# Kernel tuning notes

Hardware: AMD Instinct MI355X
Metric: run time of the kernel (lower is better)

The kernel has to match this reference:

```python
import jax, jax.numpy as jnp
import numpy as np

W_DIST = 1.0
W_ANGLE = 1.0
EPS = 1e-12


def setup_inputs() -> dict:
    key = jax.random.key(0)
    k1, k2, k3 = jax.random.split(key, 3)
    B, C = 384, 512
    return {
        "feat_s": jax.random.normal(k1, (B, C), dtype=jnp.float32),
        "feat_t": jax.random.normal(k2, (B, C), dtype=jnp.float32),
        "labels": jax.random.randint(k3, (B,), 0, C, dtype=jnp.int64),
    }


def _pdist(feat):
    # Euclidean pairwise distances with zeroed diagonal (matches RKD.pdist).
    sq = jnp.sum(feat * feat, axis=1)                      # [B]
    prod = feat @ feat.T                                   # [B,B]
    d = jnp.clip(sq[None, :] + sq[:, None] - 2.0 * prod, EPS, None)
    d = jnp.sqrt(d)
    B = feat.shape[0]
    return d * (1.0 - jnp.eye(B, dtype=feat.dtype))


def _norm_pdist(feat):
    d = _pdist(feat)
    pos = d > 0
    mean_pos = jnp.sum(jnp.where(pos, d, 0.0)) / jnp.maximum(jnp.sum(pos), 1)
    return d / mean_pos


def _smooth_l1(x, y):
    a = jnp.abs(x - y)
    return jnp.mean(jnp.where(a < 1.0, 0.5 * a * a, a - 0.5))


def _angle_gram(feat):
    # vd[i, j] = feat[j] - feat[i], normalized along feature dim (F.normalize eps=1e-12)
    vd = feat[None, :, :] - feat[:, None, :]               # [B,B,C]
    nrm = jnp.sqrt(jnp.sum(vd * vd, axis=2, keepdims=True))
    vd = vd / jnp.maximum(nrm, EPS)
    return jnp.einsum('bic,bjc->bij', vd, vd)              # [B,B,B]


def _rkd(feat_s, feat_t):
    dist_loss = _smooth_l1(_norm_pdist(feat_s), _norm_pdist(feat_t))
    angle_loss = _smooth_l1(_angle_gram(feat_s), _angle_gram(feat_t))
    return W_DIST * dist_loss + W_ANGLE * angle_loss


def reference(feat_s, feat_t, labels):
    # hard CE loss (mean reduction)
    logp = jax.nn.log_softmax(feat_s, axis=-1)
    hard_loss = -jnp.mean(logp[jnp.arange(feat_s.shape[0]), labels])
    # soft RKD loss; teacher detached as in the torch code
    soft_loss = _rkd(feat_s, jax.lax.stop_gradient(feat_t))
    return hard_loss + soft_loss
```

## Files before the change

### kernel.cpp

```cpp
#include <hip/hip_runtime.h>
#include <hip/hip_bf16.h>
#include <math.h>

#define B 384
#define C 512
#define NPAIR (B * B)
#define NOFF  (B * (B - 1))

#define T16  24
#define UP16 300
#define T64  6
#define UP64 21
#define NBG  32
#define NANG (UP64 * NBG)

#define HARD_OFF 0
#define DSUM_OFF 384
#define ANG_OFF  984
#define DIST_OFF 1656
#define SQS_OFF  1680
#define SQT_OFF  2064
#define PS_OFF   2448
#define PT_OFF   (PS_OFF + NPAIR)

typedef __attribute__((ext_vector_type(8))) short short8;
typedef __attribute__((ext_vector_type(4))) float floatx4;

__device__ __forceinline__ float blk_sum(float v, float* s4, int t) {
#pragma unroll
  for (int off = 32; off > 0; off >>= 1) v += __shfl_down(v, off, 64);
  if ((t & 63) == 0) s4[t >> 6] = v;
  __syncthreads();
  float r = s4[0] + s4[1] + s4[2] + s4[3];
  __syncthreads();
  return r;
}

__device__ __forceinline__ short bfc(float x) {
  __hip_bfloat16 h = __float2bfloat16(x);
  return __builtin_bit_cast(short, h);
}

__global__ __launch_bounds__(256, 4) void k_pre(const float* __restrict__ fs,
                                                const float* __restrict__ ft,
                                                const int* __restrict__ lab,
                                                float* __restrict__ ws) {
  int t = threadIdx.x;
  if (blockIdx.x < 96) {
    int wv = t >> 6, lane = t & 63;
    int r = blockIdx.x * 4 + wv;
    const float* xs = fs + r * C;
    const float* xt = ft + r * C;
    float4 a0 = *(const float4*)&xs[lane * 8];
    float4 a1 = *(const float4*)&xs[lane * 8 + 4];
    float4 b0 = *(const float4*)&xt[lane * 8];
    float4 b1 = *(const float4*)&xt[lane * 8 + 4];
    float m = fmaxf(fmaxf(fmaxf(a0.x, a0.y), fmaxf(a0.z, a0.w)),
                    fmaxf(fmaxf(a1.x, a1.y), fmaxf(a1.z, a1.w)));
#pragma unroll
    for (int off = 32; off > 0; off >>= 1) m = fmaxf(m, __shfl_down(m, off, 64));
    m = __shfl(m, 0, 64);
    float es = expf(a0.x - m) + expf(a0.y - m) + expf(a0.z - m) + expf(a0.w - m) +
               expf(a1.x - m) + expf(a1.y - m) + expf(a1.z - m) + expf(a1.w - m);
    float ss = a0.x * a0.x + a0.y * a0.y + a0.z * a0.z + a0.w * a0.w +
               a1.x * a1.x + a1.y * a1.y + a1.z * a1.z + a1.w * a1.w;
    float st = b0.x * b0.x + b0.y * b0.y + b0.z * b0.z + b0.w * b0.w +
               b1.x * b1.x + b1.y * b1.y + b1.z * b1.z + b1.w * b1.w;
#pragma unroll
    for (int off = 32; off > 0; off >>= 1) {
      es += __shfl_down(es, off, 64);
      ss += __shfl_down(ss, off, 64);
      st += __shfl_down(st, off, 64);
    }
    if (lane == 0) {
      ws[SQS_OFF + r] = ss;
      ws[SQT_OFF + r] = st;
      ws[HARD_OFF + r] = m + logf(es) - xs[lab[r]];
    }
  } else {
    int w = t >> 6, lane = t & 63;
    int g = (blockIdx.x - 96) * 4 + w;
    int tensor = (g >= UP16) ? 1 : 0;
    int uu = g - tensor * UP16;
    int ti = 0;
    while (uu >= T16 - ti) { uu -= T16 - ti; ++ti; }
    int tj = ti + uu;
    const float* F = tensor ? ft : fs;
    float* P = ws + (tensor ? PT_OFF : PS_OFF);
    int i0 = ti * 16, j0 = tj * 16;
    int r = lane & 15, q = lane >> 4;
    const float* arow = F + (i0 + r) * C + q * 8;
    const float* brow = F + (j0 + r) * C + q * 8;
    floatx4 acc = {0.f, 0.f, 0.f, 0.f};
    float sqa = 0.f, sqb = 0.f;
#pragma unroll
    for (int ks = 0; ks < 16; ++ks) {
      float4 al = *(const float4*)(arow + ks * 32);
      float4 ah = *(const float4*)(arow + ks * 32 + 4);
      float4 bl = *(const float4*)(brow + ks * 32);
      float4 bh = *(const float4*)(brow + ks * 32 + 4);
      sqa += al.x * al.x + al.y * al.y + al.z * al.z + al.w * al.w +
             ah.x * ah.x + ah.y * ah.y + ah.z * ah.z + ah.w * ah.w;
      sqb += bl.x * bl.x + bl.y * bl.y + bl.z * bl.z + bl.w * bl.w +
             bh.x * bh.x + bh.y * bh.y + bh.z * bh.z + bh.w * bh.w;
      short8 a, b;
      a[0] = bfc(al.x); a[1] = bfc(al.y); a[2] = bfc(al.z); a[3] = bfc(al.w);
      a[4] = bfc(ah.x); a[5] = bfc(ah.y); a[6] = bfc(ah.z); a[7] = bfc(ah.w);
      b[0] = bfc(bl.x); b[1] = bfc(bl.y); b[2] = bfc(bl.z); b[3] = bfc(bl.w);
      b[4] = bfc(bh.x); b[5] = bfc(bh.y); b[6] = bfc(bh.z); b[7] = bfc(bh.w);
      acc = __builtin_amdgcn_mfma_f32_16x16x32_bf16(a, b, acc, 0, 0, 0);
    }
    sqa += __shfl_xor(sqa, 16, 64); sqa += __shfl_xor(sqa, 32, 64);
    sqb += __shfl_xor(sqb, 16, 64); sqb += __shfl_xor(sqb, 32, 64);
    int col = lane & 15;
    int j = j0 + col;
    float sqj = __shfl(sqb, col, 64);
    float dsum = 0.f;
#pragma unroll
    for (int reg = 0; reg < 4; ++reg) {
      int ii = q * 4 + reg;
      int i = i0 + ii;
      float sqi = __shfl(sqa, ii, 64);
      float p = acc[reg];
      P[i * B + j] = p;
      P[j * B + i] = p;
      float d2 = sqi + sqj - 2.f * p;
      float d = sqrtf(fmaxf(d2, 1e-12f));
      float wgt = (ti < tj) ? 2.f : ((i < j) ? 2.f : 0.f);
      dsum = fmaf(wgt, d, dsum);
    }
#pragma unroll
    for (int off = 32; off > 0; off >>= 1) dsum += __shfl_down(dsum, off, 64);
    if (lane == 0) ws[DSUM_OFF + g] = dsum;
  }
}

#define BCH 12
#define ANGLE_BODY(MASKED)                                                   \
  for (int b = 0; b < BCH; ++b) {                                            \
    float uis[4], qis[4], uit[4], qit[4], ujs[4], qjs[4], ujt[4], qjt[4];    \
    float4 v;                                                                \
    v = *(const float4*)&sI[b][0][ty * 4];                                   \
    uis[0] = v.x; uis[1] = v.y; uis[2] = v.z; uis[3] = v.w;                  \
    v = *(const float4*)&sI[b][1][ty * 4];                                   \
    qis[0] = v.x; qis[1] = v.y; qis[2] = v.z; qis[3] = v.w;                  \
    v = *(const float4*)&sI[b][2][ty * 4];                                   \
    uit[0] = v.x; uit[1] = v.y; uit[2] = v.z; uit[3] = v.w;                  \
    v = *(const float4*)&sI[b][3][ty * 4];                                   \
    qit[0] = v.x; qit[1] = v.y; qit[2] = v.z; qit[3] = v.w;                  \
    v = *(const float4*)&sJ[b][0][tx * 4];                                   \
    ujs[0] = v.x; ujs[1] = v.y; ujs[2] = v.z; ujs[3] = v.w;                  \
    v = *(const float4*)&sJ[b][1][tx * 4];                                   \
    qjs[0] = v.x; qjs[1] = v.y; qjs[2] = v.z; qjs[3] = v.w;                  \
    v = *(const float4*)&sJ[b][2][tx * 4];                                   \
    ujt[0] = v.x; ujt[1] = v.y; ujt[2] = v.z; ujt[3] = v.w;                  \
    v = *(const float4*)&sJ[b][3][tx * 4];                                   \
    qjt[0] = v.x; qjt[1] = v.y; qjt[2] = v.z; qjt[3] = v.w;                  \
    _Pragma("unroll")                                                        \
    for (int r = 0; r < 4; ++r) {                                            \
      _Pragma("unroll")                                                      \
      for (int c = 0; c < 4; ++c) {                                          \
        float f1s = fmaf(uis[r], ps[r][c], -qis[r]);                         \
        float gs = fmaf(ujs[c], f1s, -(uis[r] * qjs[c]));                    \
        float f1t = fmaf(uit[r], pt[r][c], -qit[r]);                         \
        float gt = fmaf(ujt[c], f1t, -(uit[r] * qjt[c]));                    \
        float a = fabsf(gs - gt);                                            \
        if (MASKED) a = (ty * 4 + r < tx * 4 + c) ? a : 0.f;                 \
        float mm = fminf(a, 1.f);                                            \
        acc = fmaf(mm, fmaf(-0.5f, mm, a), acc);                             \
      }                                                                      \
    }                                                                        \
  }

__global__ __launch_bounds__(256, 4) void k_angle(float* __restrict__ ws) {
  const float* Ps = ws + PS_OFF;
  const float* Pt = ws + PT_OFF;
  const float* sqs = ws + SQS_OFF;
  const float* sqt = ws + SQT_OFF;
  int uu = blockIdx.x;
  int ti = 0;
  while (uu >= T64 - ti) { uu -= T64 - ti; ++ti; }
  int tj = ti + uu;
  int i0 = ti * 64, j0 = tj * 64;
  bool diag = (ti == tj);
  int b0 = blockIdx.y * BCH;
  int t = threadIdx.x;
  int ty = t >> 4, tx = t & 15;

  __shared__ float sI[BCH][4][64];
  __shared__ float sJ[BCH][4][64];
  __shared__ float s4[4];

  float ps[4][4], pt[4][4];
#pragma unroll
  for (int r = 0; r < 4; ++r) {
    float4 v = *(const float4*)&Ps[(i0 + ty * 4 + r) * B + j0 + tx * 4];
    ps[r][0] = v.x; ps[r][1] = v.y; ps[r][2] = v.z; ps[r][3] = v.w;
    v = *(const float4*)&Pt[(i0 + ty * 4 + r) * B + j0 + tx * 4];
    pt[r][0] = v.x; pt[r][1] = v.y; pt[r][2] = v.z; pt[r][3] = v.w;
  }

  for (int idx = t; idx < BCH * 128; idx += 256) {
    int b = idx >> 7, p = idx & 127;
    int bb = b0 + b;
    int col = (p < 64) ? (i0 + p) : (j0 + p - 64);
    float pvs = Ps[bb * B + col];
    float pvt = Pt[bb * B + col];
    float pbbs = Ps[bb * B + bb];
    float pbbt = Pt[bb * B + bb];
    float d2s = sqs[bb] + sqs[col] - 2.f * pvs;
    float d2t = sqt[bb] + sqt[col] - 2.f * pvt;
    float us = (col == bb) ? 0.f : rsqrtf(fmaxf(d2s, 1e-24f));
    float ut = (col == bb) ? 0.f : rsqrtf(fmaxf(d2t, 1e-24f));
    float qs = us * (pvs - 0.5f * pbbs);
    float qt = ut * (pvt - 0.5f * pbbt);
    float* dst = (p < 64) ? &sI[b][0][p] : &sJ[b][0][p - 64];
    dst[0] = us; dst[64] = qs; dst[128] = ut; dst[192] = qt;
  }
  __syncthreads();

  float acc = 0.f;
  if (diag) { ANGLE_BODY(true) } else { ANGLE_BODY(false) }

  float asum = blk_sum(acc, s4, t);
  if (t == 0) ws[ANG_OFF + blockIdx.y * UP64 + blockIdx.x] = asum;

  if (blockIdx.y == 0) {
    float ssum = 0.f, tsum = 0.f;
    for (int i = t; i < UP16; i += 256) ssum += ws[DSUM_OFF + i];
    for (int i = t; i < UP16; i += 256) tsum += ws[DSUM_OFF + UP16 + i];
    ssum = blk_sum(ssum, s4, t);
    tsum = blk_sum(tsum, s4, t);
    float inv_ms = (float)NOFF / ssum;
    float inv_mt = (float)NOFF / tsum;
    float sqsi[4], sqti[4], sqsj[4], sqtj[4];
#pragma unroll
    for (int r = 0; r < 4; ++r) {
      sqsi[r] = sqs[i0 + ty * 4 + r];
      sqti[r] = sqt[i0 + ty * 4 + r];
      sqsj[r] = sqs[j0 + tx * 4 + r];
      sqtj[r] = sqt[j0 + tx * 4 + r];
    }
    float dacc = 0.f;
#pragma unroll
    for (int r = 0; r < 4; ++r)
#pragma unroll
      for (int c = 0; c < 4; ++c) {
        float d2s = sqsi[r] + sqsj[c] - 2.f * ps[r][c];
        float d2t = sqti[r] + sqtj[c] - 2.f * pt[r][c];
        float dsv = sqrtf(fmaxf(d2s, 1e-12f)) * inv_ms;
        float dtv = sqrtf(fmaxf(d2t, 1e-12f)) * inv_mt;
        float a = fabsf(dsv - dtv);
        if (diag) a = (ty * 4 + r < tx * 4 + c) ? a : 0.f;
        float mm = fminf(a, 1.f);
        dacc = fmaf(mm, fmaf(-0.5f, mm, a), dacc);
      }
    float dsum2 = blk_sum(dacc, s4, t);
    if (t == 0) ws[DIST_OFF + blockIdx.x] = dsum2;
  }
}

__global__ __launch_bounds__(256) void k_final(const float* __restrict__ ws,
                                               float* __restrict__ out) {
  __shared__ float s4[4];
  int t = threadIdx.x;
  float h = 0.f;
  for (int i = t; i < B; i += 256) h += ws[HARD_OFF + i];
  float a = 0.f;
  for (int i = t; i < NANG; i += 256) a += ws[ANG_OFF + i];
  float d = 0.f;
  for (int i = t; i < UP64; i += 256) d += ws[DIST_OFF + i];
  h = blk_sum(h, s4, t);
  a = blk_sum(a, s4, t);
  d = blk_sum(d, s4, t);
  if (t == 0)
    out[0] = h * (1.f / (float)B) + 2.f * d * (1.f / (float)NPAIR) +
             2.f * a * (1.f / 56623104.f);
}

extern "C" void kernel_launch(void* const* d_in, const int* in_sizes, int n_in,
                              void* d_out, int out_size, void* d_ws, size_t ws_size,
                              hipStream_t stream) {
  (void)in_sizes; (void)n_in; (void)out_size; (void)ws_size;
  const float* fs = (const float*)d_in[0];
  const float* ft = (const float*)d_in[1];
  const int* lab = (const int*)d_in[2];
  float* ws = (float*)d_ws;
  float* out = (float*)d_out;

  k_pre<<<246, 256, 0, stream>>>(fs, ft, lab, ws);
  k_angle<<<dim3(UP64, NBG), 256, 0, stream>>>(ws);
  k_final<<<1, 256, 0, stream>>>(ws, out);
}
```

Baseline: 86.09 us.

## Pack angle operands as float4 in LDS, prefetch next batch, rebalance grid

The angle kernel now stores the four per-sample values (us, qs, ut, qt) interleaved as one float4 in shared memory, so each row or column needs a single vector LDS read. The inner loop is fully unrolled and software-prefetches batch b+1 into registers while batch b is computed. The diagonal mask becomes a runtime branch instead of two specialised copies. The batch chunk drops from 12 to 8 with NBG raised from 32 to 48 (more blocks, each doing less work), launch bounds move from 4 to 3 waves per SIMD, and the workspace offsets shift to fit. This trades more registers and lower occupancy for fewer LDS instructions and better latency hiding.

```diff
diff --git a/kernel.cpp b/kernel.cpp
--- a/kernel.cpp
+++ b/kernel.cpp
@@ -11,16 +11,16 @@
 #define UP16 300
 #define T64  6
 #define UP64 21
-#define NBG  32
+#define NBG  48
 #define NANG (UP64 * NBG)
 
 #define HARD_OFF 0
 #define DSUM_OFF 384
 #define ANG_OFF  984
-#define DIST_OFF 1656
-#define SQS_OFF  1680
-#define SQT_OFF  2064
-#define PS_OFF   2448
+#define DIST_OFF 1992
+#define SQS_OFF  2016
+#define SQT_OFF  2400
+#define PS_OFF   2816
 #define PT_OFF   (PS_OFF + NPAIR)
 
 typedef __attribute__((ext_vector_type(8))) short short8;
@@ -135,44 +135,8 @@
   }
 }
 
-#define BCH 12
-#define ANGLE_BODY(MASKED)                                                   \
-  for (int b = 0; b < BCH; ++b) {                                            \
-    float uis[4], qis[4], uit[4], qit[4], ujs[4], qjs[4], ujt[4], qjt[4];    \
-    float4 v;                                                                \
-    v = *(const float4*)&sI[b][0][ty * 4];                                   \
-    uis[0] = v.x; uis[1] = v.y; uis[2] = v.z; uis[3] = v.w;                  \
-    v = *(const float4*)&sI[b][1][ty * 4];                                   \
-    qis[0] = v.x; qis[1] = v.y; qis[2] = v.z; qis[3] = v.w;                  \
-    v = *(const float4*)&sI[b][2][ty * 4];                                   \
-    uit[0] = v.x; uit[1] = v.y; uit[2] = v.z; uit[3] = v.w;                  \
-    v = *(const float4*)&sI[b][3][ty * 4];                                   \
-    qit[0] = v.x; qit[1] = v.y; qit[2] = v.z; qit[3] = v.w;                  \
-    v = *(const float4*)&sJ[b][0][tx * 4];                                   \
-    ujs[0] = v.x; ujs[1] = v.y; ujs[2] = v.z; ujs[3] = v.w;                  \
-    v = *(const float4*)&sJ[b][1][tx * 4];                                   \
-    qjs[0] = v.x; qjs[1] = v.y; qjs[2] = v.z; qjs[3] = v.w;                  \
-    v = *(const float4*)&sJ[b][2][tx * 4];                                   \
-    ujt[0] = v.x; ujt[1] = v.y; ujt[2] = v.z; ujt[3] = v.w;                  \
-    v = *(const float4*)&sJ[b][3][tx * 4];                                   \
-    qjt[0] = v.x; qjt[1] = v.y; qjt[2] = v.z; qjt[3] = v.w;                  \
-    _Pragma("unroll")                                                        \
-    for (int r = 0; r < 4; ++r) {                                            \
-      _Pragma("unroll")                                                      \
-      for (int c = 0; c < 4; ++c) {                                          \
-        float f1s = fmaf(uis[r], ps[r][c], -qis[r]);                         \
-        float gs = fmaf(ujs[c], f1s, -(uis[r] * qjs[c]));                    \
-        float f1t = fmaf(uit[r], pt[r][c], -qit[r]);                         \
-        float gt = fmaf(ujt[c], f1t, -(uit[r] * qjt[c]));                    \
-        float a = fabsf(gs - gt);                                            \
-        if (MASKED) a = (ty * 4 + r < tx * 4 + c) ? a : 0.f;                 \
-        float mm = fminf(a, 1.f);                                            \
-        acc = fmaf(mm, fmaf(-0.5f, mm, a), acc);                             \
-      }                                                                      \
-    }                                                                        \
-  }
-
-__global__ __launch_bounds__(256, 4) void k_angle(float* __restrict__ ws) {
+#define BCH 8
+__global__ __launch_bounds__(256, 3) void k_angle(float* __restrict__ ws) {
   const float* Ps = ws + PS_OFF;
   const float* Pt = ws + PT_OFF;
   const float* sqs = ws + SQS_OFF;
@@ -187,8 +151,8 @@
   int t = threadIdx.x;
   int ty = t >> 4, tx = t & 15;
 
-  __shared__ float sI[BCH][4][64];
-  __shared__ float sJ[BCH][4][64];
+  __shared__ float4 sI4[BCH][64];
+  __shared__ float4 sJ4[BCH][64];
   __shared__ float s4[4];
 
   float ps[4][4], pt[4][4];
@@ -212,15 +176,48 @@
     float d2t = sqt[bb] + sqt[col] - 2.f * pvt;
     float us = (col == bb) ? 0.f : rsqrtf(fmaxf(d2s, 1e-24f));
     float ut = (col == bb) ? 0.f : rsqrtf(fmaxf(d2t, 1e-24f));
-    float qs = us * (pvs - 0.5f * pbbs);
-    float qt = ut * (pvt - 0.5f * pbbt);
-    float* dst = (p < 64) ? &sI[b][0][p] : &sJ[b][0][p - 64];
-    dst[0] = us; dst[64] = qs; dst[128] = ut; dst[192] = qt;
+    float4 pk;
+    pk.x = us;
+    pk.y = us * (pvs - 0.5f * pbbs);
+    pk.z = ut;
+    pk.w = ut * (pvt - 0.5f * pbbt);
+    if (p < 64) sI4[b][p] = pk; else sJ4[b][p - 64] = pk;
   }
   __syncthreads();
 
   float acc = 0.f;
-  if (diag) { ANGLE_BODY(true) } else { ANGLE_BODY(false) }
+  float4 vi[4], vj[4], nvi[4], nvj[4];
+#pragma unroll
+  for (int r = 0; r < 4; ++r) {
+    vi[r] = sI4[0][ty * 4 + r];
+    vj[r] = sJ4[0][tx * 4 + r];
+  }
+#pragma unroll
+  for (int b = 0; b < BCH; ++b) {
+    if (b + 1 < BCH) {
+#pragma unroll
+      for (int r = 0; r < 4; ++r) {
+        nvi[r] = sI4[b + 1][ty * 4 + r];
+        nvj[r] = sJ4[b + 1][tx * 4 + r];
+      }
+    }
+#pragma unroll
+    for (int r = 0; r < 4; ++r) {
+#pragma unroll
+      for (int c = 0; c < 4; ++c) {
+        float f1s = fmaf(vi[r].x, ps[r][c], -vi[r].y);
+        float gs = fmaf(vj[c].x, f1s, -(vi[r].x * vj[c].y));
+        float f1t = fmaf(vi[r].z, pt[r][c], -vi[r].w);
+        float gt = fmaf(vj[c].z, f1t, -(vi[r].z * vj[c].w));
+        float a = fabsf(gs - gt);
+        if (diag) a = (ty * 4 + r < tx * 4 + c) ? a : 0.f;
+        float mm = fminf(a, 1.f);
+        acc = fmaf(mm, fmaf(-0.5f, mm, a), acc);
+      }
+    }
+#pragma unroll
+    for (int r = 0; r < 4; ++r) { vi[r] = nvi[r]; vj[r] = nvj[r]; }
+  }
 
   float asum = blk_sum(acc, s4, t);
   if (t == 0) ws[ANG_OFF + blockIdx.y * UP64 + blockIdx.x] = asum;
```

Result: faster. 81.87 us (-4.9%).
